# Optimization experiments

Hardware: AMD Instinct MI355X
Metric: run time of the kernel (lower is better)

Reference implementation:

```python
import jax, jax.numpy as jnp
import numpy as np

B_DIM, C_DIM, K_DIM, L_DIM = 16, 64, 207, 64
SUPPORT_LEN, ORDER = 2, 2
C_IN = (ORDER * SUPPORT_LEN + 1) * C_DIM  # 320, include_self=True


def setup_inputs() -> dict:
    key = jax.random.key(0)
    k1, k2, k3, k4 = jax.random.split(key, 4)
    x = jax.random.normal(k1, (B_DIM, C_DIM, K_DIM * L_DIM), dtype=jnp.float32)
    # per-batch adaptive adjacencies (B, K, K), nonnegative like softmax(relu(E1 E2^T))
    a0 = jax.random.uniform(k2, (B_DIM, K_DIM, K_DIM), dtype=jnp.float32)
    a1 = jax.random.uniform(k3, (B_DIM, K_DIM, K_DIM), dtype=jnp.float32)
    # 1x1 conv weight (C_out, C_in) and bias
    W = jax.random.normal(k4, (C_DIM, C_IN), dtype=jnp.float32) * (1.0 / np.sqrt(C_IN))
    b = jnp.zeros((C_DIM,), dtype=jnp.float32)
    return {"x": x, "a0": a0, "a1": a1, "W": W, "b": b, "K": K_DIM, "L": L_DIM}


def reference(x, a0, a1, W, b, K, L):
    B, C = x.shape[0], x.shape[1]
    x = x.reshape(B, C, K, L)  # (B, C, K, L)
    # torch: x1[bl, c, j] = sum_k x[bl, c, k] * a[b, j, k]  (bmm with a^T)
    diffuse = lambda h, a: jnp.einsum('bckl,bjk->bcjl', h, a)
    out = [x]  # include_self=True
    for a in (a0, a1):
        x1 = diffuse(x, a)
        out.append(x1)
        for _ in range(2, ORDER + 1):
            x1 = diffuse(x1, a)
            out.append(x1)
    h = jnp.concatenate(out, axis=1)  # (B, 5C, K, L)
    y = jnp.einsum('bikl,oi->bokl', h, W) + b[None, :, None, None]  # 1x1 conv
    return y.reshape(B, C, K * L)
```

## Files before the change

### kernel.cpp

```cpp
#include <hip/hip_runtime.h>

typedef unsigned short u16;
typedef __bf16 bf16x8 __attribute__((ext_vector_type(8)));
typedef float f32x4 __attribute__((ext_vector_type(4)));

#define NB 16
#define NC 64
#define NK 207
#define NL 64
#define KP 224
#define NKL 13248
#define CIN 320


__device__ __forceinline__ u16 f2bf(float f) {
  unsigned u = __builtin_bit_cast(unsigned, f);
  u += 0x7FFFu + ((u >> 16) & 1u);
  return (u16)(u >> 16);
}

__device__ __forceinline__ void g2l16(const u16* gsrc, u16* ldst) {
  __builtin_amdgcn_global_load_lds(
      (const __attribute__((address_space(1))) unsigned int*)gsrc,
      (__attribute__((address_space(3))) unsigned int*)ldst, 16, 0, 0);
}

__global__ __launch_bounds__(256) void k_prep(
    const float* __restrict__ x, const float* __restrict__ a0,
    const float* __restrict__ a1, const float* __restrict__ W,
    u16* __restrict__ Xf, u16* __restrict__ Af, u16* __restrict__ Atf,
    u16* __restrict__ Gf, u16* __restrict__ Wbf) {
  __shared__ __align__(16) u16 xs[16 * 2048];
  int id = blockIdx.x, t = threadIdx.x;
  if (id < 512) {
    int b = id >> 5, rem = id & 31;
    int c4 = rem >> 3, lh = (rem >> 1) & 3, ksh = rem & 1;
    int ks0 = ksh ? 4 : 0, nks = ksh ? 3 : 4;
    int kw = nks * 32;
    int l0 = lh * 16;
    int cl = t >> 4, kl = t & 15;
    const float* xc = x + (size_t)(b * 64 + c4 * 16 + cl) * NKL;
    for (int kk = kl; kk < kw; kk += 16) {
      int k = ksh * 128 + kk;
      float4 v0 = {0.f, 0.f, 0.f, 0.f}, v1 = v0, v2 = v0, v3 = v0;
      if (k < NK) {
        const float4* p = (const float4*)(xc + (size_t)k * 64 + l0);
        v0 = p[0]; v1 = p[1]; v2 = p[2]; v3 = p[3];
      }
      int ksl = kk >> 5, q = (kk >> 3) & 3, e = kk & 7;
      u16* dst = &xs[ksl * 512 + (cl + 16 * q) * 8 + e];
      dst[0 * 2048] = f2bf(v0.x);  dst[1 * 2048] = f2bf(v0.y);
      dst[2 * 2048] = f2bf(v0.z);  dst[3 * 2048] = f2bf(v0.w);
      dst[4 * 2048] = f2bf(v1.x);  dst[5 * 2048] = f2bf(v1.y);
      dst[6 * 2048] = f2bf(v1.z);  dst[7 * 2048] = f2bf(v1.w);
      dst[8 * 2048] = f2bf(v2.x);  dst[9 * 2048] = f2bf(v2.y);
      dst[10 * 2048] = f2bf(v2.z); dst[11 * 2048] = f2bf(v2.w);
      dst[12 * 2048] = f2bf(v3.x); dst[13 * 2048] = f2bf(v3.y);
      dst[14 * 2048] = f2bf(v3.z); dst[15 * 2048] = f2bf(v3.w);
    }
    __syncthreads();
    int wavei = t >> 6, lane = t & 63;
    u16* Xb = Xf + (size_t)b * 256 * 7 * 512;
    for (int ll = wavei; ll < 16; ll += 4) {
      int l = l0 + ll;
      for (int ksl = 0; ksl < nks; ksl++) {
        bf16x8 v = *(const bf16x8*)&xs[ll * 2048 + ksl * 512 + lane * 8];
        *(bf16x8*)(Xb + ((size_t)(l * 4 + c4) * 7 + ks0 + ksl) * 512 +
                   lane * 8) = v;
      }
    }
  } else if (id < 800) {
    int local = id - 512;
    int rt = local % 9, bw = local / 9;
    int b = bw >> 1, w = bw & 1;
    const float* A = (w ? a1 : a0) + (size_t)b * NK * NK;
    u16* Ab = Af + (size_t)bw * 16 * 7 * 512;
    u16* Gp = Gf + ((size_t)b * 5 + (1 + 2 * w)) * 13 * 7 * 512;
    if (rt == 8) {
      int4 z = {0, 0, 0, 0};
      int4* p = (int4*)(Ab + (size_t)14 * 7 * 512);
      for (int ci = t; ci < 896; ci += 256) p[ci] = z;
    } else {
      int m0 = rt * 28;
      int kc = t & 31, rl = t >> 5;
      if (kc < 28) {
#pragma unroll
        for (int i = 0; i < 4; i++) {
          int ml = rl + 8 * i;
          if (ml < 28) {
            int m = m0 + ml;
            u16 v[8] __attribute__((aligned(16)));
#pragma unroll
            for (int j = 0; j < 8; j++) {
              int k = kc * 8 + j;
              v[j] = (m < NK && k < NK) ? f2bf(A[m * NK + k]) : (u16)0;
            }
            size_t fo = ((size_t)(m >> 4) * 7 + (kc >> 2)) * 512 +
                        ((m & 15) + 16 * (kc & 3)) * 8;
            *(int4*)(Ab + fo) = *(int4*)v;
            if (m < 208) *(int4*)(Gp + fo) = *(int4*)v;
          }
        }
      }
    }
  } else if (id < 1024) {
    int local = id - 800;
    int g = local % 7, bw = local / 7;
    int b = bw >> 1, w = bw & 1;
    const float* A = (w ? a1 : a0) + (size_t)b * NK * NK;
    u16* At = Atf + (size_t)bw * 16 * 7 * 512;
    int n = t;
#pragma unroll
    for (int mc4 = 0; mc4 < 4; mc4++) {
      int mc = g * 4 + mc4;
      u16 v[8] __attribute__((aligned(16)));
#pragma unroll
      for (int j = 0; j < 8; j++) {
        int m = mc * 8 + j;
        v[j] = (n < NK && m < NK) ? f2bf(A[m * NK + n]) : (u16)0;
      }
      *(int4*)(At + ((size_t)(n >> 4) * 7 + (mc >> 2)) * 512 +
               ((n & 15) + 16 * (mc & 3)) * 8) = *(int4*)v;
    }
  } else if (id < 1056) {
    int local = id - 1024, b = local >> 1, half = local & 1;
    u16* Gp = Gf + (size_t)b * 5 * 13 * 7 * 512;
    for (int ci = t; ci < 104 * 28; ci += 256) {
      int jr = ci / 28, kc = ci - jr * 28;
      int j = half * 104 + jr;
      u16 v[8] __attribute__((aligned(16)));
      for (int jj = 0; jj < 8; jj++)
        v[jj] = (j == kc * 8 + jj && j < NK) ? (u16)0x3F80 : (u16)0;
      *(int4*)(Gp + ((size_t)(j >> 4) * 7 + (kc >> 2)) * 512 +
               ((j & 15) + 16 * (kc & 3)) * 8) = *(int4*)v;
    }
  } else {
    for (int ci = t; ci < 2560; ci += 256) {
      int o = ci / 40, kc = ci - o * 40;
      u16 v[8] __attribute__((aligned(16)));
      for (int j = 0; j < 8; j++) v[j] = f2bf(W[o * CIN + kc * 8 + j]);
      *(int4*)(Wbf + ((size_t)(o >> 4) * 10 + (kc >> 2)) * 512 +
               ((o & 15) + 16 * (kc & 3)) * 8) = *(int4*)v;
    }
  }
}

__global__ __launch_bounds__(256) void k_asq(
    const u16* __restrict__ Af, const u16* __restrict__ Atf,
    u16* __restrict__ Gf) {
  int b = blockIdx.z >> 1, w = blockIdx.z & 1;
  int lane = threadIdx.x & 63, wave = threadIdx.x >> 6;
  int wm = wave >> 1, wn = wave & 1;
  const u16* Ab = Af + ((size_t)b * 2 + w) * 16 * 7 * 512;
  const u16* At = Atf + ((size_t)b * 2 + w) * 16 * 7 * 512;
  int m0 = blockIdx.y * 64 + wm * 32;
  int n0 = blockIdx.x * 64 + wn * 32;
  int r = lane & 15, q = lane >> 4;
  f32x4 acc[2][2] = {};
#pragma unroll
  for (int ks = 0; ks < 7; ks++) {
    bf16x8 af[2], bg[2];
    for (int i = 0; i < 2; i++)
      af[i] = *(const bf16x8*)(Ab + ((size_t)((m0 >> 4) + i) * 7 + ks) * 512 + lane * 8);
    for (int i = 0; i < 2; i++)
      bg[i] = *(const bf16x8*)(At + ((size_t)((n0 >> 4) + i) * 7 + ks) * 512 + lane * 8);
    for (int i = 0; i < 2; i++)
      for (int j = 0; j < 2; j++)
        acc[i][j] = __builtin_amdgcn_mfma_f32_16x16x32_bf16(af[i], bg[j], acc[i][j], 0, 0, 0);
  }
  int qblk = 2 + 2 * w;
  u16* Gp = Gf + ((size_t)b * 5 + qblk) * 13 * 7 * 512;
  for (int i = 0; i < 2; i++)
    for (int j = 0; j < 2; j++)
      for (int rr = 0; rr < 4; rr++) {
        int mj = m0 + i * 16 + q * 4 + rr;
        int nk = n0 + j * 16 + r;
        if (mj < 208 && nk < KP)
          Gp[((size_t)(mj >> 4) * 7 + (nk >> 5)) * 512 +
             ((mj & 15) + 16 * ((nk >> 3) & 3)) * 8 + (nk & 7)] = f2bf(acc[i][j][rr]);
      }
}

#define AG 17920
__global__ __launch_bounds__(512, 4) void k_fused(
    const u16* __restrict__ Gf, const u16* __restrict__ Xf,
    const u16* __restrict__ Wbf, const float* __restrict__ bias,
    float* __restrict__ y) {
  __shared__ __align__(16) u16 lds[AG + 2 * 8192];
  int id = blockIdx.x;
  int wg = (id & 7) * 416 + (id >> 3);
  int b = wg / 208, rem = wg % 208;
  int jt = rem >> 4, lt = rem & 15;
  int tid = threadIdx.x, wave = tid >> 6, lane = tid & 63;
  int r = lane & 15, q = lane >> 4;
  const u16* Gb = Gf + (size_t)b * 5 * 13 * 7 * 512;
  const u16* Xw = Xf + ((size_t)b * 256 + lt * 16) * 7 * 512;

  for (int i2 = 0; i2 < 5; i2++) {
    int tile = i2 * 8 + wave;
    if (tile < 35) {
      int p = tile / 7, ks = tile - p * 7;
      g2l16(Gb + ((size_t)(p * 13 + jt) * 7 + ks) * 512 + lane * 8,
            &lds[tile * 512 + lane * 8]);
    }
  }
  for (int i2 = 0; i2 < 2; i2++) {
    int tl = wave * 2 + i2;
    g2l16(Xw + (size_t)tl * 7 * 512 + lane * 8, &lds[AG + tl * 512 + lane * 8]);
  }
  asm volatile("s_waitcnt vmcnt(2)" ::: "memory");
  __builtin_amdgcn_s_barrier();

  f32x4 acc1[5][2] = {};
#pragma unroll
  for (int ks = 0; ks < 7; ks++) {
    int cur = ks & 1;
    if (ks < 6) {
      for (int i2 = 0; i2 < 2; i2++) {
        int tl = wave * 2 + i2;
        g2l16(Xw + ((size_t)tl * 7 + ks + 1) * 512 + lane * 8,
              &lds[AG + (cur ^ 1) * 8192 + tl * 512 + lane * 8]);
      }
      asm volatile("s_waitcnt vmcnt(2)" ::: "memory");
    } else {
      asm volatile("s_waitcnt vmcnt(0)" ::: "memory");
    }
    bf16x8 af0 = *(const bf16x8*)&lds[AG + cur * 8192 + (wave * 2 + 0) * 512 + lane * 8];
    bf16x8 af1 = *(const bf16x8*)&lds[AG + cur * 8192 + (wave * 2 + 1) * 512 + lane * 8];
    __builtin_amdgcn_s_setprio(1);
#pragma unroll
    for (int p = 0; p < 5; p++) {
      bf16x8 bg = *(const bf16x8*)&lds[(p * 7 + ks) * 512 + lane * 8];
      acc1[p][0] = __builtin_amdgcn_mfma_f32_16x16x32_bf16(af0, bg, acc1[p][0], 0, 0, 0);
      acc1[p][1] = __builtin_amdgcn_mfma_f32_16x16x32_bf16(af1, bg, acc1[p][1], 0, 0, 0);
    }
    __builtin_amdgcn_s_setprio(0);
  }
  __syncthreads();

#pragma unroll
  for (int p = 0; p < 5; p++)
#pragma unroll
    for (int mf = 0; mf < 2; mf++) {
      int m = (wave * 2 + mf) * 16 + q * 4;
      int tt = m >> 6, c = m & 63;
      int cs = c ^ ((r & 7) << 3);
      int idxT = ((p * 16 + r) * 4 + tt) * 72 + cs;
      u16 v0 = f2bf(acc1[p][mf][0]), v1 = f2bf(acc1[p][mf][1]);
      u16 v2 = f2bf(acc1[p][mf][2]), v3 = f2bf(acc1[p][mf][3]);
      *(uint2*)&lds[idxT] = make_uint2((unsigned)v0 | ((unsigned)v1 << 16),
                                       (unsigned)v2 | ((unsigned)v3 << 16));
    }
  int mo = wave >> 1, nh = (wave & 1) * 2;
  const u16* Wt = Wbf + (size_t)mo * 10 * 512 + lane * 8;
  bf16x8 aw[10];
#pragma unroll
  for (int ks = 0; ks < 10; ks++) aw[ks] = *(const bf16x8*)(Wt + ks * 512);
  __syncthreads();

  f32x4 acc2[2] = {};
#pragma unroll
  for (int ks = 0; ks < 10; ks++) {
    int p = ks >> 1, c0 = (ks & 1) * 32;
#pragma unroll
    for (int nf = 0; nf < 2; nf++) {
      int n = (nh + nf) * 16 + r;
      int j = n >> 2, tt = n & 3;
      int cs = (c0 + q * 8) ^ ((j & 7) << 3);
      bf16x8 bt = *(const bf16x8*)&lds[((p * 16 + j) * 4 + tt) * 72 + cs];
      acc2[nf] = __builtin_amdgcn_mfma_f32_16x16x32_bf16(aw[ks], bt, acc2[nf], 0, 0, 0);
    }
  }

  int o0 = mo * 16 + q * 4;
  float4 bv = *(const float4*)&bias[o0];
  float* yb = y + (size_t)b * 64 * NKL;
#pragma unroll
  for (int nf = 0; nf < 2; nf++) {
    int n = (nh + nf) * 16 + r;
    int j = n >> 2, tt = n & 3;
    int jnode = jt * 16 + j;
    if (jnode < NK) {
      int col = jnode * 64 + lt * 4 + tt;
      yb[(size_t)(o0 + 0) * NKL + col] = acc2[nf][0] + bv.x;
      yb[(size_t)(o0 + 1) * NKL + col] = acc2[nf][1] + bv.y;
      yb[(size_t)(o0 + 2) * NKL + col] = acc2[nf][2] + bv.z;
      yb[(size_t)(o0 + 3) * NKL + col] = acc2[nf][3] + bv.w;
    }
  }
}

extern "C" void kernel_launch(void* const* d_in, const int* in_sizes, int n_in,
                              void* d_out, int out_size, void* d_ws, size_t ws_size,
                              hipStream_t stream) {
  const float* x = (const float*)d_in[0];
  const float* a0 = (const float*)d_in[1];
  const float* a1 = (const float*)d_in[2];
  const float* W = (const float*)d_in[3];
  const float* bias = (const float*)d_in[4];
  float* y = (float*)d_out;
  char* ws = (char*)d_ws;

  size_t off = 0;
  auto alloc = [&](size_t bytes) {
    size_t o = off;
    off = (off + bytes + 511) & ~(size_t)511;
    return o;
  };
  size_t o_Xf = alloc((size_t)NB * 256 * 7 * 512 * 2);
  size_t o_Gf = alloc((size_t)NB * 5 * 13 * 7 * 512 * 2);
  size_t o_Af = alloc((size_t)NB * 2 * 16 * 7 * 512 * 2);
  size_t o_At = alloc((size_t)NB * 2 * 16 * 7 * 512 * 2);
  size_t o_Wf = alloc((size_t)4 * 10 * 512 * 2);
  (void)ws_size;

  u16* Xf  = (u16*)(ws + o_Xf);
  u16* Gf  = (u16*)(ws + o_Gf);
  u16* Af  = (u16*)(ws + o_Af);
  u16* Atf = (u16*)(ws + o_At);
  u16* Wf  = (u16*)(ws + o_Wf);

  k_prep<<<dim3(1057), 256, 0, stream>>>(x, a0, a1, W, Xf, Af, Atf, Gf, Wf);
  k_asq<<<dim3(4, 4, 32), 256, 0, stream>>>(Af, Atf, Gf);
  k_fused<<<dim3(16 * 13 * 16), 512, 0, stream>>>(Gf, Xf, Wf, bias, y);
}
```

Before: 189.4 us.

## Fuse adjacency conversion and A² computation into one per-matrix LDS kernel

Moves adjacency bf16 conversion, identity block generation and the A·A product into a new kernel that runs one workgroup per (batch, adjacency), stages A and column chunks of A in LDS, and computes A² with MFMA straight from shared memory. This removes the Af/Atf global intermediates and the separate k_asq launch. The x/W prep is split into its own kernel. Only 32 workgroups now carry the A work, with large LDS use and scalar strided transposed global reads, so that stage has far less parallelism.

```diff
diff --git a/kernel.cpp b/kernel.cpp
--- a/kernel.cpp
+++ b/kernel.cpp
@@ -25,11 +25,9 @@
       (__attribute__((address_space(3))) unsigned int*)ldst, 16, 0, 0);
 }
 
-__global__ __launch_bounds__(256) void k_prep(
-    const float* __restrict__ x, const float* __restrict__ a0,
-    const float* __restrict__ a1, const float* __restrict__ W,
-    u16* __restrict__ Xf, u16* __restrict__ Af, u16* __restrict__ Atf,
-    u16* __restrict__ Gf, u16* __restrict__ Wbf) {
+__global__ __launch_bounds__(256) void k_prepx(
+    const float* __restrict__ x, const float* __restrict__ W,
+    u16* __restrict__ Xf, u16* __restrict__ Wbf) {
   __shared__ __align__(16) u16 xs[16 * 2048];
   int id = blockIdx.x, t = threadIdx.x;
   if (id < 512) {
@@ -69,71 +67,6 @@
                    lane * 8) = v;
       }
     }
-  } else if (id < 800) {
-    int local = id - 512;
-    int rt = local % 9, bw = local / 9;
-    int b = bw >> 1, w = bw & 1;
-    const float* A = (w ? a1 : a0) + (size_t)b * NK * NK;
-    u16* Ab = Af + (size_t)bw * 16 * 7 * 512;
-    u16* Gp = Gf + ((size_t)b * 5 + (1 + 2 * w)) * 13 * 7 * 512;
-    if (rt == 8) {
-      int4 z = {0, 0, 0, 0};
-      int4* p = (int4*)(Ab + (size_t)14 * 7 * 512);
-      for (int ci = t; ci < 896; ci += 256) p[ci] = z;
-    } else {
-      int m0 = rt * 28;
-      int kc = t & 31, rl = t >> 5;
-      if (kc < 28) {
-#pragma unroll
-        for (int i = 0; i < 4; i++) {
-          int ml = rl + 8 * i;
-          if (ml < 28) {
-            int m = m0 + ml;
-            u16 v[8] __attribute__((aligned(16)));
-#pragma unroll
-            for (int j = 0; j < 8; j++) {
-              int k = kc * 8 + j;
-              v[j] = (m < NK && k < NK) ? f2bf(A[m * NK + k]) : (u16)0;
-            }
-            size_t fo = ((size_t)(m >> 4) * 7 + (kc >> 2)) * 512 +
-                        ((m & 15) + 16 * (kc & 3)) * 8;
-            *(int4*)(Ab + fo) = *(int4*)v;
-            if (m < 208) *(int4*)(Gp + fo) = *(int4*)v;
-          }
-        }
-      }
-    }
-  } else if (id < 1024) {
-    int local = id - 800;
-    int g = local % 7, bw = local / 7;
-    int b = bw >> 1, w = bw & 1;
-    const float* A = (w ? a1 : a0) + (size_t)b * NK * NK;
-    u16* At = Atf + (size_t)bw * 16 * 7 * 512;
-    int n = t;
-#pragma unroll
-    for (int mc4 = 0; mc4 < 4; mc4++) {
-      int mc = g * 4 + mc4;
-      u16 v[8] __attribute__((aligned(16)));
-#pragma unroll
-      for (int j = 0; j < 8; j++) {
-        int m = mc * 8 + j;
-        v[j] = (n < NK && m < NK) ? f2bf(A[m * NK + n]) : (u16)0;
-      }
-      *(int4*)(At + ((size_t)(n >> 4) * 7 + (mc >> 2)) * 512 +
-               ((n & 15) + 16 * (mc & 3)) * 8) = *(int4*)v;
-    }
-  } else if (id < 1056) {
-    int local = id - 1024, b = local >> 1, half = local & 1;
-    u16* Gp = Gf + (size_t)b * 5 * 13 * 7 * 512;
-    for (int ci = t; ci < 104 * 28; ci += 256) {
-      int jr = ci / 28, kc = ci - jr * 28;
-      int j = half * 104 + jr;
-      u16 v[8] __attribute__((aligned(16)));
-      for (int jj = 0; jj < 8; jj++)
-        v[jj] = (j == kc * 8 + jj && j < NK) ? (u16)0x3F80 : (u16)0;
-      *(int4*)(Gp + ((size_t)(j >> 4) * 7 + (kc >> 2)) * 512 +
-               ((j & 15) + 16 * (kc & 3)) * 8) = *(int4*)v;
-    }
   } else {
     for (int ci = t; ci < 2560; ci += 256) {
       int o = ci / 40, kc = ci - o * 40;
@@ -145,40 +78,87 @@
   }
 }
 
-__global__ __launch_bounds__(256) void k_asq(
-    const u16* __restrict__ Af, const u16* __restrict__ Atf,
+#define ACOL 50176
+__global__ __launch_bounds__(512) void k_prepa(
+    const float* __restrict__ a0, const float* __restrict__ a1,
     u16* __restrict__ Gf) {
-  int b = blockIdx.z >> 1, w = blockIdx.z & 1;
-  int lane = threadIdx.x & 63, wave = threadIdx.x >> 6;
-  int wm = wave >> 1, wn = wave & 1;
-  const u16* Ab = Af + ((size_t)b * 2 + w) * 16 * 7 * 512;
-  const u16* At = Atf + ((size_t)b * 2 + w) * 16 * 7 * 512;
-  int m0 = blockIdx.y * 64 + wm * 32;
-  int n0 = blockIdx.x * 64 + wn * 32;
+  __shared__ __align__(16) u16 al[64512];
+  int bw = blockIdx.x;
+  int b = bw >> 1, w = bw & 1;
+  int t = threadIdx.x;
+  int wave = t >> 6, lane = t & 63;
   int r = lane & 15, q = lane >> 4;
-  f32x4 acc[2][2] = {};
-#pragma unroll
-  for (int ks = 0; ks < 7; ks++) {
-    bf16x8 af[2], bg[2];
-    for (int i = 0; i < 2; i++)
-      af[i] = *(const bf16x8*)(Ab + ((size_t)((m0 >> 4) + i) * 7 + ks) * 512 + lane * 8);
-    for (int i = 0; i < 2; i++)
-      bg[i] = *(const bf16x8*)(At + ((size_t)((n0 >> 4) + i) * 7 + ks) * 512 + lane * 8);
-    for (int i = 0; i < 2; i++)
-      for (int j = 0; j < 2; j++)
-        acc[i][j] = __builtin_amdgcn_mfma_f32_16x16x32_bf16(af[i], bg[j], acc[i][j], 0, 0, 0);
-  }
-  int qblk = 2 + 2 * w;
-  u16* Gp = Gf + ((size_t)b * 5 + qblk) * 13 * 7 * 512;
-  for (int i = 0; i < 2; i++)
-    for (int j = 0; j < 2; j++)
+  const float* A = (w ? a1 : a0) + (size_t)b * NK * NK;
+
+  for (int u = t; u < 6272; u += 512) {
+    int m = u / 28, kc = u - m * 28;
+    u16 v[8] __attribute__((aligned(16)));
+#pragma unroll
+    for (int j = 0; j < 8; j++) {
+      int k = kc * 8 + j;
+      v[j] = (m < NK && k < NK) ? f2bf(A[(size_t)m * NK + k]) : (u16)0;
+    }
+    *(int4*)&al[((m >> 4) * 7 + (kc >> 2)) * 512 +
+                ((m & 15) + 16 * (kc & 3)) * 8] = *(int4*)v;
+  }
+  __syncthreads();
+
+  u16* Gp13 = Gf + ((size_t)b * 5 + 1 + 2 * w) * 13 * 7 * 512;
+  for (int f = wave; f < 91; f += 8) {
+    bf16x8 v = *(const bf16x8*)&al[(size_t)f * 512 + lane * 8];
+    *(bf16x8*)(Gp13 + (size_t)f * 512 + lane * 8) = v;
+  }
+
+  if (w == 0) {
+    u16* Gp0 = Gf + (size_t)b * 5 * 13 * 7 * 512;
+    for (int u = t; u < 91 * 64; u += 512) {
+      int f = u >> 6, pos = u & 63;
+      int jt = f / 7, ks = f - jt * 7;
+      int j = jt * 16 + (pos & 15), qq = pos >> 4;
+      u16 v[8] __attribute__((aligned(16)));
+#pragma unroll
+      for (int e = 0; e < 8; e++) {
+        int k = ks * 32 + qq * 8 + e;
+        v[e] = (j == k && j < NK) ? (u16)0x3F80 : (u16)0;
+      }
+      *(int4*)(Gp0 + (size_t)f * 512 + pos * 8) = *(int4*)v;
+    }
+  }
+
+  u16* Gp24 = Gf + ((size_t)b * 5 + 2 + 2 * w) * 13 * 7 * 512;
+  for (int ch = 0; ch < 4; ch++) {
+    int n0 = ch * 64;
+    __syncthreads();
+    {
+      int n = n0 + lane;
+      for (int mi = 0; mi < 28; mi++) {
+        int m = wave * 28 + mi;
+        u16 v = (n < NK && m < NK) ? f2bf(A[(size_t)m * NK + n]) : (u16)0;
+        al[ACOL + ((lane >> 4) * 7 + (m >> 5)) * 512 +
+           ((lane & 15) + 16 * ((m >> 3) & 3)) * 8 + (m & 7)] = v;
+      }
+    }
+    __syncthreads();
+    for (int o = wave; o < 56; o += 8) {
+      int mt = o >> 2, nt = o & 3;
+      f32x4 acc = {};
+#pragma unroll
+      for (int ks = 0; ks < 7; ks++) {
+        bf16x8 af = *(const bf16x8*)&al[(mt * 7 + ks) * 512 + lane * 8];
+        bf16x8 bg = *(const bf16x8*)&al[ACOL + (nt * 7 + ks) * 512 + lane * 8];
+        acc = __builtin_amdgcn_mfma_f32_16x16x32_bf16(af, bg, acc, 0, 0, 0);
+      }
+#pragma unroll
       for (int rr = 0; rr < 4; rr++) {
-        int mj = m0 + i * 16 + q * 4 + rr;
-        int nk = n0 + j * 16 + r;
+        int mj = mt * 16 + q * 4 + rr;
+        int nk = n0 + nt * 16 + r;
         if (mj < 208 && nk < KP)
-          Gp[((size_t)(mj >> 4) * 7 + (nk >> 5)) * 512 +
-             ((mj & 15) + 16 * ((nk >> 3) & 3)) * 8 + (nk & 7)] = f2bf(acc[i][j][rr]);
-      }
+          Gp24[((size_t)(mj >> 4) * 7 + (nk >> 5)) * 512 +
+               ((mj & 15) + 16 * ((nk >> 3) & 3)) * 8 + (nk & 7)] =
+              f2bf(acc[rr]);
+      }
+    }
+  }
 }
 
 #define AG 17920
@@ -309,18 +289,14 @@
   };
   size_t o_Xf = alloc((size_t)NB * 256 * 7 * 512 * 2);
   size_t o_Gf = alloc((size_t)NB * 5 * 13 * 7 * 512 * 2);
-  size_t o_Af = alloc((size_t)NB * 2 * 16 * 7 * 512 * 2);
-  size_t o_At = alloc((size_t)NB * 2 * 16 * 7 * 512 * 2);
   size_t o_Wf = alloc((size_t)4 * 10 * 512 * 2);
   (void)ws_size;
 
-  u16* Xf  = (u16*)(ws + o_Xf);
-  u16* Gf  = (u16*)(ws + o_Gf);
-  u16* Af  = (u16*)(ws + o_Af);
-  u16* Atf = (u16*)(ws + o_At);
-  u16* Wf  = (u16*)(ws + o_Wf);
-
-  k_prep<<<dim3(1057), 256, 0, stream>>>(x, a0, a1, W, Xf, Af, Atf, Gf, Wf);
-  k_asq<<<dim3(4, 4, 32), 256, 0, stream>>>(Af, Atf, Gf);
+  u16* Xf = (u16*)(ws + o_Xf);
+  u16* Gf = (u16*)(ws + o_Gf);
+  u16* Wf = (u16*)(ws + o_Wf);
+
+  k_prepa<<<dim3(32), 512, 0, stream>>>(a0, a1, Gf);
+  k_prepx<<<dim3(513), 256, 0, stream>>>(x, W, Xf, Wf);
   k_fused<<<dim3(16 * 13 * 16), 512, 0, stream>>>(Gf, Xf, Wf, bias, y);
 }
```

New measurement: 222.1 us. 17.2% more time.
